# Kernel tuning notes

Hardware: AMD Instinct MI355X
Metric: run time of the kernel (lower is better)

The kernel has to match this reference:

```python
import jax, jax.numpy as jnp
import numpy as np

NEG_BIG = -9e15
ALPHA = 0.2  # leaky relu slope


def setup_inputs() -> dict:
    key = jax.random.key(0)
    k1, k2, k3, k4 = jax.random.split(key, 4)
    B, N, F_in, F_out = 4, 4096, 256, 128
    h = jax.random.normal(k1, (B, N, F_in), dtype=jnp.float32)
    adj = jax.random.randint(k2, (B, N, N), 0, 2, dtype=jnp.int32)
    W = jax.random.normal(k3, (F_in, F_out), dtype=jnp.float32) * (1.0 / np.sqrt(F_in))
    a = jax.random.normal(k4, (2 * F_out,), dtype=jnp.float32) * (1.0 / np.sqrt(2 * F_out))
    return {"h": h, "adj": adj, "W": W, "a": a}


def reference(h, adj, W, a):
    F_out = W.shape[1]
    Wh = jnp.einsum("bnf,fo->bno", h, W)                    # [B,N,F_out]
    # split-a trick: a^T [Wh_i ; Wh_j] = a1.Wh_i + a2.Wh_j (same math as concat)
    f1 = Wh @ a[:F_out]                                       # [B,N] source (row) term
    f2 = Wh @ a[F_out:]                                       # [B,N] target (col) term
    e = jax.nn.leaky_relu(f1[:, :, None] + f2[:, None, :], negative_slope=ALPHA)
    e = jnp.where(adj > 0, e, NEG_BIG)
    attention = jax.nn.softmax(e, axis=-1)                   # [B,N,N]
    h_prime = jnp.einsum("bnm,bmo->bno", attention, Wh)      # [B,N,F_out]
    return jax.nn.elu(h_prime)
```

## Files before the change

kernel.cpp:

```cpp
#include <hip/hip_runtime.h>
#include <hip/hip_bf16.h>

#define B_ 4
#define N_ 4096
#define FIN 256
#define FOUT 128

typedef unsigned short u16;
typedef unsigned int u32;
typedef short bf16x8 __attribute__((ext_vector_type(8)));
typedef float f32x4 __attribute__((ext_vector_type(4)));
typedef int i32x4 __attribute__((ext_vector_type(4)));

__device__ __forceinline__ u16 f2bf(float x) {
  union { float f; unsigned int u; } v;
  v.f = x;
  unsigned int r = v.u + 0x7fffu + ((v.u >> 16) & 1u);
  return (u16)(r >> 16);
}

__device__ __forceinline__ unsigned int pk2(float a, float b) {
  union { __hip_bfloat162 h2; unsigned int u; } v;
  v.h2 = __float22bfloat162_rn(make_float2(a, b));
  return v.u;
}

__global__ __launch_bounds__(256) void wh_kernel(
    const float* __restrict__ h, const float* __restrict__ W,
    const float* __restrict__ a, u16* __restrict__ whT,
    float* __restrict__ f1, float* __restrict__ f2) {
  __shared__ float hs[16 * FIN];
  const int tid = threadIdx.x;
  const int b = blockIdx.x >> 8;
  const int n0 = (blockIdx.x & 255) << 4;

  {
    const float4* src = (const float4*)(h + ((size_t)(b * N_ + n0)) * FIN);
    float4* dst = (float4*)hs;
#pragma unroll
    for (int i = 0; i < 4; ++i) dst[tid + i * 256] = src[tid + i * 256];
  }
  __syncthreads();

  const int o0 = (tid & 31) * 4;
  const int r0 = tid >> 5;
  float acc0[4] = {0.f, 0.f, 0.f, 0.f};
  float acc1[4] = {0.f, 0.f, 0.f, 0.f};
  const float* hr0 = hs + r0 * FIN;
  const float* hr1 = hs + (r0 + 8) * FIN;
#pragma unroll 4
  for (int k = 0; k < FIN; ++k) {
    const float4 w = *(const float4*)(W + k * FOUT + o0);
    const float h0 = hr0[k];
    const float h1 = hr1[k];
    acc0[0] = fmaf(h0, w.x, acc0[0]); acc0[1] = fmaf(h0, w.y, acc0[1]);
    acc0[2] = fmaf(h0, w.z, acc0[2]); acc0[3] = fmaf(h0, w.w, acc0[3]);
    acc1[0] = fmaf(h1, w.x, acc1[0]); acc1[1] = fmaf(h1, w.y, acc1[1]);
    acc1[2] = fmaf(h1, w.z, acc1[2]); acc1[3] = fmaf(h1, w.w, acc1[3]);
  }

  float s10 = 0.f, s11 = 0.f, s20 = 0.f, s21 = 0.f;
#pragma unroll
  for (int j = 0; j < 4; ++j) {
    const float a1v = a[o0 + j];
    const float a2v = a[FOUT + o0 + j];
    s10 = fmaf(acc0[j], a1v, s10); s20 = fmaf(acc0[j], a2v, s20);
    s11 = fmaf(acc1[j], a1v, s11); s21 = fmaf(acc1[j], a2v, s21);
  }
#pragma unroll
  for (int off = 16; off >= 1; off >>= 1) {
    s10 += __shfl_xor(s10, off); s11 += __shfl_xor(s11, off);
    s20 += __shfl_xor(s20, off); s21 += __shfl_xor(s21, off);
  }
  if ((tid & 31) == 0) {
    const int base = b * N_ + n0;
    f1[base + r0] = s10; f1[base + r0 + 8] = s11;
    f2[base + r0] = s20; f2[base + r0 + 8] = s21;
  }

  __syncthreads();
  u16* ts = (u16*)hs;
#pragma unroll
  for (int j = 0; j < 4; ++j) {
    ts[(o0 + j) * 16 + r0]     = f2bf(acc0[j]);
    ts[(o0 + j) * 16 + r0 + 8] = f2bf(acc1[j]);
  }
  __syncthreads();
  const int o  = tid >> 1;
  const int hh = tid & 1;
  const uint4 vals = *(const uint4*)(ts + o * 16 + hh * 8);
  u16* dst = whT + ((size_t)((b * 512 + (n0 >> 3) + hh) * 128 + o)) * 8;
  *(uint4*)dst = vals;
}

__global__ __launch_bounds__(256) void pack_kernel(
    const int* __restrict__ adj, u32* __restrict__ pw) {
  const size_t gid = (size_t)blockIdx.x * 256 + threadIdx.x;
  const i32x4* src = (const i32x4*)(adj + gid * 32);
  u32 m = 0;
#pragma unroll
  for (int c = 0; c < 8; ++c) {
    const i32x4 v = __builtin_nontemporal_load(src + c);
    m |= (v[0] > 0 ? 1u : 0u) << (c * 4 + 0);
    m |= (v[1] > 0 ? 1u : 0u) << (c * 4 + 1);
    m |= (v[2] > 0 ? 1u : 0u) << (c * 4 + 2);
    m |= (v[3] > 0 ? 1u : 0u) << (c * 4 + 3);
  }
  pw[gid] = m;
}

__device__ __forceinline__ float pv2(u32 bit, float t) {
  const float e = fmaxf(t, 0.2f * t);
  const float ex = __expf(e);
  return bit ? ex : 0.f;
}

__global__ __launch_bounds__(256) void gat_kernel(
    const u32* __restrict__ pw, const u16* __restrict__ whT,
    const float* __restrict__ f1, const float* __restrict__ f2,
    float* __restrict__ out) {
  __shared__ float red[9360];
  const int tid = threadIdx.x;
  const int wave = tid >> 6;
  const int lane = tid & 63;
  const int b = blockIdx.x >> 8;
  const int i0 = (blockIdx.x & 255) << 4;
  const int row = lane & 15;
  const int kg = lane >> 4;
  const int j0 = wave << 10;
  const int ksh = kg << 3;

  const float f1r = f1[b * N_ + i0 + row];
  const u32* mp = pw + ((size_t)(b * N_ + i0 + row)) * 128 + wave * 32;
  const float4* fp = (const float4*)(f2 + b * N_ + j0 + (kg << 3));
  const u16* wp = whT + ((size_t)((b * 512 + (j0 >> 3) + kg) * 128 + row)) * 8;

  f32x4 acc[9];
#pragma unroll
  for (int i = 0; i < 9; ++i) acc[i] = (f32x4){0.f, 0.f, 0.f, 0.f};
  bf16x8 ones;
#pragma unroll
  for (int i = 0; i < 8; ++i) ones[i] = (short)0x3F80;

  auto compute = [&](u32 mw, float4 fa, float4 fb) {
    bf16x8 bf0 = *(const bf16x8*)(wp);
    bf16x8 bf1 = *(const bf16x8*)(wp + 128);
    bf16x8 bf2 = *(const bf16x8*)(wp + 256);
    bf16x8 bf3 = *(const bf16x8*)(wp + 384);
    bf16x8 bf4 = *(const bf16x8*)(wp + 512);
    bf16x8 bf5 = *(const bf16x8*)(wp + 640);
    bf16x8 bf6 = *(const bf16x8*)(wp + 768);
    bf16x8 bf7 = *(const bf16x8*)(wp + 896);
    const u32 mb = mw >> ksh;
    const float p0 = pv2(mb & 1u,        f1r + fa.x);
    const float p1 = pv2((mb >> 1) & 1u, f1r + fa.y);
    const float p2 = pv2((mb >> 2) & 1u, f1r + fa.z);
    const float p3 = pv2((mb >> 3) & 1u, f1r + fa.w);
    const float p4 = pv2((mb >> 4) & 1u, f1r + fb.x);
    const float p5 = pv2((mb >> 5) & 1u, f1r + fb.y);
    const float p6 = pv2((mb >> 6) & 1u, f1r + fb.z);
    const float p7 = pv2((mb >> 7) & 1u, f1r + fb.w);
    union { bf16x8 v; unsigned int u[4]; } pf;
    pf.u[0] = pk2(p0, p1); pf.u[1] = pk2(p2, p3);
    pf.u[2] = pk2(p4, p5); pf.u[3] = pk2(p6, p7);
    __builtin_amdgcn_s_setprio(1);
    acc[0] = __builtin_amdgcn_mfma_f32_16x16x32_bf16(pf.v, bf0, acc[0], 0, 0, 0);
    acc[1] = __builtin_amdgcn_mfma_f32_16x16x32_bf16(pf.v, bf1, acc[1], 0, 0, 0);
    acc[2] = __builtin_amdgcn_mfma_f32_16x16x32_bf16(pf.v, bf2, acc[2], 0, 0, 0);
    acc[3] = __builtin_amdgcn_mfma_f32_16x16x32_bf16(pf.v, bf3, acc[3], 0, 0, 0);
    acc[4] = __builtin_amdgcn_mfma_f32_16x16x32_bf16(pf.v, bf4, acc[4], 0, 0, 0);
    acc[5] = __builtin_amdgcn_mfma_f32_16x16x32_bf16(pf.v, bf5, acc[5], 0, 0, 0);
    acc[6] = __builtin_amdgcn_mfma_f32_16x16x32_bf16(pf.v, bf6, acc[6], 0, 0, 0);
    acc[7] = __builtin_amdgcn_mfma_f32_16x16x32_bf16(pf.v, bf7, acc[7], 0, 0, 0);
    acc[8] = __builtin_amdgcn_mfma_f32_16x16x32_bf16(pf.v, ones, acc[8], 0, 0, 0);
    __builtin_amdgcn_s_setprio(0);
    wp += 4096;
  };

  u32 m_0 = mp[0];
  float4 fa_0 = fp[0], fb_0 = fp[1];
  u32 m_1 = mp[1];
  float4 fa_1 = fp[8], fb_1 = fp[9];

  for (int s = 0; s < 15; ++s) {
    u32 nm = mp[2 * s + 2];
    float4 nfa = fp[16 * s + 16], nfb = fp[16 * s + 17];
    compute(m_0, fa_0, fb_0);
    m_0 = nm; fa_0 = nfa; fb_0 = nfb;

    nm = mp[2 * s + 3];
    nfa = fp[16 * s + 24]; nfb = fp[16 * s + 25];
    compute(m_1, fa_1, fb_1);
    m_1 = nm; fa_1 = nfa; fb_1 = nfb;
  }
  compute(m_0, fa_0, fb_0);
  compute(m_1, fa_1, fb_1);

#pragma unroll
  for (int fi = 0; fi < 9; ++fi)
    *(f32x4*)&red[(wave * 9 + fi) * 260 + lane * 4] = acc[fi];
  __syncthreads();

  const int i = tid >> 4;
  const int oo = (tid & 15) * 8;
  const int lnb = (i >> 2) << 4;
  const int rg = i & 3;
  float lt = 0.f;
#pragma unroll
  for (int w = 0; w < 4; ++w) lt += red[(w * 9 + 8) * 260 + lnb * 4 + rg];
  const float inv = 1.f / lt;
  float res[8];
#pragma unroll
  for (int jo = 0; jo < 8; ++jo) {
    const int o = oo + jo;
    const int fi = o >> 4;
    const int lidx = lnb + (o & 15);
    float sacc = 0.f;
#pragma unroll
    for (int w = 0; w < 4; ++w)
      sacc += red[(w * 9 + fi) * 260 + lidx * 4 + rg];
    const float x = sacc * inv;
    res[jo] = x > 0.f ? x : expm1f(x);
  }
  float4* op = (float4*)(out + ((size_t)(b * N_ + i0 + i)) * FOUT + oo);
  op[0] = make_float4(res[0], res[1], res[2], res[3]);
  op[1] = make_float4(res[4], res[5], res[6], res[7]);
}

extern "C" void kernel_launch(void* const* d_in, const int* in_sizes, int n_in,
                              void* d_out, int out_size, void* d_ws, size_t ws_size,
                              hipStream_t stream) {
  const float* h = (const float*)d_in[0];
  const int* adj = (const int*)d_in[1];
  const float* W = (const float*)d_in[2];
  const float* a = (const float*)d_in[3];
  float* out = (float*)d_out;

  char* wsb = (char*)d_ws;
  u16* whT = (u16*)wsb;
  float* f1 = (float*)(wsb + (size_t)B_ * FOUT * N_ * sizeof(u16));
  float* f2 = f1 + B_ * N_;
  u32* pw = (u32*)(wsb + (size_t)B_ * FOUT * N_ * sizeof(u16)
                   + 2 * (size_t)B_ * N_ * sizeof(float));

  pack_kernel<<<dim3(B_ * N_ * 128 / 256), dim3(256), 0, stream>>>(adj, pw);
  wh_kernel<<<dim3(B_ * (N_ / 16)), dim3(256), 0, stream>>>(h, W, a, whT, f1, f2);
  gat_kernel<<<dim3(B_ * (N_ / 16)), dim3(256), 0, stream>>>(pw, whT, f1, f2, out);
}
```

Before: 498.4 us.

## Split GAT output features across waves instead of splitting neighbor range

Each wave now loops over all 4096 neighbors but owns only 32 of the 128 output columns, computing 2 feature MFMAs plus the row-sum MFMA per step. This removes the shared-memory cross-wave reduction and the block barrier, and writes output directly from accumulators. In exchange each wave recomputes the masked exponentials for the full row (4x redundant exp/mask work and mask/f2 loads), and the register prefetch pipeline and setprio are dropped.

```diff
diff --git a/kernel.cpp b/kernel.cpp
--- a/kernel.cpp
+++ b/kernel.cpp
@@ -119,39 +119,34 @@
     const u32* __restrict__ pw, const u16* __restrict__ whT,
     const float* __restrict__ f1, const float* __restrict__ f2,
     float* __restrict__ out) {
-  __shared__ float red[9360];
   const int tid = threadIdx.x;
-  const int wave = tid >> 6;
+  const int w = tid >> 6;
   const int lane = tid & 63;
   const int b = blockIdx.x >> 8;
   const int i0 = (blockIdx.x & 255) << 4;
   const int row = lane & 15;
   const int kg = lane >> 4;
-  const int j0 = wave << 10;
   const int ksh = kg << 3;
 
   const float f1r = f1[b * N_ + i0 + row];
-  const u32* mp = pw + ((size_t)(b * N_ + i0 + row)) * 128 + wave * 32;
-  const float4* fp = (const float4*)(f2 + b * N_ + j0 + (kg << 3));
-  const u16* wp = whT + ((size_t)((b * 512 + (j0 >> 3) + kg) * 128 + row)) * 8;
-
-  f32x4 acc[9];
-#pragma unroll
-  for (int i = 0; i < 9; ++i) acc[i] = (f32x4){0.f, 0.f, 0.f, 0.f};
+  const u32* mp = pw + ((size_t)(b * N_ + i0 + row)) * 128;
+  const float4* fq = (const float4*)(f2 + b * N_) + 2 * kg;
+  const u16* wp = whT + ((size_t)((b * 512 + kg) * 128 + 32 * w + row)) * 8;
+
+  f32x4 accA = (f32x4){0.f, 0.f, 0.f, 0.f};
+  f32x4 accB = (f32x4){0.f, 0.f, 0.f, 0.f};
+  f32x4 accD = (f32x4){0.f, 0.f, 0.f, 0.f};
   bf16x8 ones;
 #pragma unroll
   for (int i = 0; i < 8; ++i) ones[i] = (short)0x3F80;
 
-  auto compute = [&](u32 mw, float4 fa, float4 fb) {
-    bf16x8 bf0 = *(const bf16x8*)(wp);
-    bf16x8 bf1 = *(const bf16x8*)(wp + 128);
-    bf16x8 bf2 = *(const bf16x8*)(wp + 256);
-    bf16x8 bf3 = *(const bf16x8*)(wp + 384);
-    bf16x8 bf4 = *(const bf16x8*)(wp + 512);
-    bf16x8 bf5 = *(const bf16x8*)(wp + 640);
-    bf16x8 bf6 = *(const bf16x8*)(wp + 768);
-    bf16x8 bf7 = *(const bf16x8*)(wp + 896);
-    const u32 mb = mw >> ksh;
+#pragma unroll 2
+  for (int s = 0; s < 128; ++s) {
+    const bf16x8 bfA = *(const bf16x8*)(wp);
+    const bf16x8 bfB = *(const bf16x8*)(wp + 128);
+    const u32 mb = mp[s] >> ksh;
+    const float4 fa = fq[0];
+    const float4 fb = fq[1];
     const float p0 = pv2(mb & 1u,        f1r + fa.x);
     const float p1 = pv2((mb >> 1) & 1u, f1r + fa.y);
     const float p2 = pv2((mb >> 2) & 1u, f1r + fa.z);
@@ -163,68 +158,24 @@
     union { bf16x8 v; unsigned int u[4]; } pf;
     pf.u[0] = pk2(p0, p1); pf.u[1] = pk2(p2, p3);
     pf.u[2] = pk2(p4, p5); pf.u[3] = pk2(p6, p7);
-    __builtin_amdgcn_s_setprio(1);
-    acc[0] = __builtin_amdgcn_mfma_f32_16x16x32_bf16(pf.v, bf0, acc[0], 0, 0, 0);
-    acc[1] = __builtin_amdgcn_mfma_f32_16x16x32_bf16(pf.v, bf1, acc[1], 0, 0, 0);
-    acc[2] = __builtin_amdgcn_mfma_f32_16x16x32_bf16(pf.v, bf2, acc[2], 0, 0, 0);
-    acc[3] = __builtin_amdgcn_mfma_f32_16x16x32_bf16(pf.v, bf3, acc[3], 0, 0, 0);
-    acc[4] = __builtin_amdgcn_mfma_f32_16x16x32_bf16(pf.v, bf4, acc[4], 0, 0, 0);
-    acc[5] = __builtin_amdgcn_mfma_f32_16x16x32_bf16(pf.v, bf5, acc[5], 0, 0, 0);
-    acc[6] = __builtin_amdgcn_mfma_f32_16x16x32_bf16(pf.v, bf6, acc[6], 0, 0, 0);
-    acc[7] = __builtin_amdgcn_mfma_f32_16x16x32_bf16(pf.v, bf7, acc[7], 0, 0, 0);
-    acc[8] = __builtin_amdgcn_mfma_f32_16x16x32_bf16(pf.v, ones, acc[8], 0, 0, 0);
-    __builtin_amdgcn_s_setprio(0);
+    accA = __builtin_amdgcn_mfma_f32_16x16x32_bf16(pf.v, bfA, accA, 0, 0, 0);
+    accB = __builtin_amdgcn_mfma_f32_16x16x32_bf16(pf.v, bfB, accB, 0, 0, 0);
+    accD = __builtin_amdgcn_mfma_f32_16x16x32_bf16(pf.v, ones, accD, 0, 0, 0);
+    fq += 8;
     wp += 4096;
-  };
-
-  u32 m_0 = mp[0];
-  float4 fa_0 = fp[0], fb_0 = fp[1];
-  u32 m_1 = mp[1];
-  float4 fa_1 = fp[8], fb_1 = fp[9];
-
-  for (int s = 0; s < 15; ++s) {
-    u32 nm = mp[2 * s + 2];
-    float4 nfa = fp[16 * s + 16], nfb = fp[16 * s + 17];
-    compute(m_0, fa_0, fb_0);
-    m_0 = nm; fa_0 = nfa; fb_0 = nfb;
-
-    nm = mp[2 * s + 3];
-    nfa = fp[16 * s + 24]; nfb = fp[16 * s + 25];
-    compute(m_1, fa_1, fb_1);
-    m_1 = nm; fa_1 = nfa; fb_1 = nfb;
-  }
-  compute(m_0, fa_0, fb_0);
-  compute(m_1, fa_1, fb_1);
-
-#pragma unroll
-  for (int fi = 0; fi < 9; ++fi)
-    *(f32x4*)&red[(wave * 9 + fi) * 260 + lane * 4] = acc[fi];
-  __syncthreads();
-
-  const int i = tid >> 4;
-  const int oo = (tid & 15) * 8;
-  const int lnb = (i >> 2) << 4;
-  const int rg = i & 3;
-  float lt = 0.f;
-#pragma unroll
-  for (int w = 0; w < 4; ++w) lt += red[(w * 9 + 8) * 260 + lnb * 4 + rg];
-  const float inv = 1.f / lt;
-  float res[8];
-#pragma unroll
-  for (int jo = 0; jo < 8; ++jo) {
-    const int o = oo + jo;
-    const int fi = o >> 4;
-    const int lidx = lnb + (o & 15);
-    float sacc = 0.f;
-#pragma unroll
-    for (int w = 0; w < 4; ++w)
-      sacc += red[(w * 9 + fi) * 260 + lidx * 4 + rg];
-    const float x = sacc * inv;
-    res[jo] = x > 0.f ? x : expm1f(x);
-  }
-  float4* op = (float4*)(out + ((size_t)(b * N_ + i0 + i)) * FOUT + oo);
-  op[0] = make_float4(res[0], res[1], res[2], res[3]);
-  op[1] = make_float4(res[4], res[5], res[6], res[7]);
+  }
+
+  const int orow = (lane >> 4) << 2;
+  const int ocol = lane & 15;
+  float* ob = out + ((size_t)(b * N_ + i0 + orow)) * FOUT + 32 * w + ocol;
+#pragma unroll
+  for (int r = 0; r < 4; ++r) {
+    const float inv = 1.f / accD[r];
+    const float xa = accA[r] * inv;
+    const float xb = accB[r] * inv;
+    ob[(size_t)r * FOUT]      = xa > 0.f ? xa : expm1f(xa);
+    ob[(size_t)r * FOUT + 16] = xb > 0.f ? xb : expm1f(xb);
+  }
 }
 
 extern "C" void kernel_launch(void* const* d_in, const int* in_sizes, int n_in,
```

After: 551.2 us. 1.11x slower.
